# Optimization experiments

Hardware: AMD Instinct MI355X
Metric: run time of the kernel (lower is better)

## Reference

```python
import jax, jax.numpy as jnp
import numpy as np

OFFSET_SCALE = 6.0
H = W = 256


def setup_inputs() -> dict:
    key = jax.random.key(0)
    k1, k2, k3, k4 = jax.random.split(key, 4)
    B = 128
    Offset = jax.random.normal(k1, (B, 3, H, W), dtype=jnp.float32) * 0.05
    Posmap_kpt = jax.random.normal(k2, (B, 3, H, W), dtype=jnp.float32)
    mean_posmap = jax.random.normal(k3, (3, H, W), dtype=jnp.float32)
    uv_kpt = jax.random.randint(k4, (68, 2), 0, H)
    return {"Offset": Offset, "Posmap_kpt": Posmap_kpt,
            "mean_posmap": mean_posmap, "uv_kpt": uv_kpt}


def _safe_norm(d):
    # row-wise L2 norm with zero-safe gradient (row 0 of d is exactly zero)
    sq = jnp.sum(d * d, axis=1)
    pos = sq > 0
    return jnp.where(pos, jnp.sqrt(jnp.where(pos, sq, 1.0)), 0.0)


def _kabsch(src, dst):
    # src, dst: [68, 3] -> similarity transform (scaled R [3,3], t [3])
    s1 = jnp.sum(_safe_norm(src - src[0]))
    s2 = jnp.sum(_safe_norm(dst - dst[0]))
    scale = s2 / s1
    A = src * scale
    AA = A - A.mean(axis=0)
    BB = dst - dst.mean(axis=0)
    Hm = AA.T @ BB                        # [3,3] cross-covariance
    U, S, Vh = jnp.linalg.svd(Hm, full_matrices=False)
    R = Vh.T @ U.T                        # torch.svd returns V, so R = V U^T
    t = jnp.mean(dst - A @ R.T, axis=0)
    return R * scale, t


def reference(Offset, Posmap_kpt, mean_posmap, uv_kpt):
    B = Offset.shape[0]
    offsetmap = (Offset * OFFSET_SCALE + mean_posmap).transpose(0, 2, 3, 1)  # [B,H,W,3]
    kptmap = Posmap_kpt.transpose(0, 2, 3, 1)                                # [B,H,W,3]
    kpt_dst = kptmap[:, uv_kpt[:, 0], uv_kpt[:, 1]]                          # [B,68,3]
    kpt_src = offsetmap[:, uv_kpt[:, 0], uv_kpt[:, 1]]                       # [B,68,3]
    offsetflat = offsetmap.reshape(B, H * W, 3)                              # [B,65536,3]
    R, t = jax.vmap(_kabsch)(kpt_src, kpt_dst)                               # [B,3,3], [B,3]
    outpos = jnp.einsum('bnd,bed->bne', offsetflat, R) + t[:, None, :]       # x @ R^T + t
    return outpos.reshape(B, H, W, 3).transpose(0, 3, 1, 2)
```

## Files before the change

### kernel.cpp

```cpp
#include <hip/hip_runtime.h>

#define HW (256*256)
#define NKPT 68
#define NB 128

typedef float v4f __attribute__((ext_vector_type(4)));

__device__ inline void inv3x3(const double m[9], double inv[9], double* detOut) {
    double c00 =  m[4]*m[8] - m[5]*m[7];
    double c01 = -(m[3]*m[8] - m[5]*m[6]);
    double c02 =  m[3]*m[7] - m[4]*m[6];
    double det = m[0]*c00 + m[1]*c01 + m[2]*c02;
    double id = 1.0 / det;
    inv[0] = c00 * id;
    inv[1] = (m[2]*m[7] - m[1]*m[8]) * id;
    inv[2] = (m[1]*m[5] - m[2]*m[4]) * id;
    inv[3] = c01 * id;
    inv[4] = (m[0]*m[8] - m[2]*m[6]) * id;
    inv[5] = (m[2]*m[3] - m[0]*m[5]) * id;
    inv[6] = c02 * id;
    inv[7] = (m[1]*m[6] - m[0]*m[7]) * id;
    inv[8] = (m[0]*m[4] - m[1]*m[3]) * id;
    *detOut = det;
}

__global__ __launch_bounds__(128) void kabsch_kernel(
    const float* __restrict__ Offset,
    const float* __restrict__ Posmap,
    const float* __restrict__ meanp,
    const int*   __restrict__ uv,
    float* __restrict__ RT)
{
    const int b   = blockIdx.x;
    const int tid = threadIdx.x;
    __shared__ double red[17][NKPT];
    __shared__ double res[17];

    if (tid < NKPT) {
        const int r  = uv[2*tid],   c  = uv[2*tid+1];
        const int r0 = uv[0],       c0 = uv[1];
        const int p  = r  * 256 + c;
        const int p0 = r0 * 256 + c0;
        const float* offB = Offset + (size_t)b * 3 * HW;
        const float* posB = Posmap + (size_t)b * 3 * HW;
        double s[3], d[3], s0[3], d0[3];
        #pragma unroll
        for (int k = 0; k < 3; ++k) {
            s[k]  = (double)offB[k*HW + p ] * 6.0 + (double)meanp[k*HW + p ];
            d[k]  = (double)posB[k*HW + p ];
            s0[k] = (double)offB[k*HW + p0] * 6.0 + (double)meanp[k*HW + p0];
            d0[k] = (double)posB[k*HW + p0];
        }
        int q = 0;
        #pragma unroll
        for (int k = 0; k < 3; ++k) red[q++][tid] = s[k];
        #pragma unroll
        for (int k = 0; k < 3; ++k) red[q++][tid] = d[k];
        #pragma unroll
        for (int i = 0; i < 3; ++i)
            #pragma unroll
            for (int j = 0; j < 3; ++j) red[q++][tid] = s[i] * d[j];
        double ns2 = 0.0, nd2 = 0.0;
        #pragma unroll
        for (int k = 0; k < 3; ++k) {
            double e = s[k] - s0[k]; ns2 += e*e;
            double f = d[k] - d0[k]; nd2 += f*f;
        }
        red[q++][tid] = (ns2 > 0.0) ? sqrt(ns2) : 0.0;
        red[q++][tid] = (nd2 > 0.0) ? sqrt(nd2) : 0.0;
    }
    __syncthreads();
    if (tid < 17) {
        double acc = 0.0;
        for (int i = 0; i < NKPT; ++i) acc += red[tid][i];
        res[tid] = acc;
    }
    __syncthreads();
    if (tid == 0) {
        const double sumS[3] = {res[0], res[1], res[2]};
        const double sumD[3] = {res[3], res[4], res[5]};
        double cross[9];
        #pragma unroll
        for (int k = 0; k < 9; ++k) cross[k] = res[6+k];
        const double s1 = res[15], s2 = res[16];
        const double scale = s2 / s1;
        double mS[3], mD[3];
        #pragma unroll
        for (int k = 0; k < 3; ++k) { mS[k] = sumS[k] / NKPT; mD[k] = sumD[k] / NKPT; }
        double Wm[9];
        #pragma unroll
        for (int i = 0; i < 3; ++i)
            #pragma unroll
            for (int j = 0; j < 3; ++j)
                Wm[i*3+j] = scale * (cross[i*3+j] - (double)NKPT * mS[i] * mD[j]);
        for (int it = 0; it < 8; ++it) {
            double inv[9], det;
            inv3x3(Wm, inv, &det);
            double g  = cbrt(fabs(det));
            double gi = 1.0 / g;
            double Wn[9];
            #pragma unroll
            for (int r = 0; r < 3; ++r)
                #pragma unroll
                for (int c = 0; c < 3; ++c)
                    Wn[r*3+c] = 0.5 * (gi * Wm[r*3+c] + g * inv[c*3+r]);
            #pragma unroll
            for (int k = 0; k < 9; ++k) Wm[k] = Wn[k];
        }
        float* o = RT + b * 12;
        #pragma unroll
        for (int e = 0; e < 3; ++e)
            #pragma unroll
            for (int d = 0; d < 3; ++d)
                o[e*3+d] = (float)(scale * Wm[d*3+e]);
        #pragma unroll
        for (int e = 0; e < 3; ++e) {
            double acc = mD[e];
            #pragma unroll
            for (int d = 0; d < 3; ++d) acc -= scale * mS[d] * Wm[d*3+e];
            o[9+e] = (float)acc;
        }
    }
}

__global__ __launch_bounds__(256) void apply_kernel(
    const float* __restrict__ Offset,
    const float* __restrict__ meanp,
    const float* __restrict__ RT,
    float* __restrict__ out)
{
    const int blk  = blockIdx.x;
    const int b    = blk >> 4;
    const int slab = blk & 15;
    const int p0   = slab * 4096 + threadIdx.x * 4;

    const float* rt = RT + b * 12;
    const float r00 = rt[0], r01 = rt[1], r02 = rt[2];
    const float r10 = rt[3], r11 = rt[4], r12 = rt[5];
    const float r20 = rt[6], r21 = rt[7], r22 = rt[8];
    const float t0  = rt[9], t1  = rt[10], t2 = rt[11];

    const size_t bbase = (size_t)b * 3 * HW;

    v4f a[3][4], m[3][4];
    #pragma unroll
    for (int g = 0; g < 4; ++g) {
        const int p = p0 + g * 1024;
        #pragma unroll
        for (int ch = 0; ch < 3; ++ch)
            a[ch][g] = __builtin_nontemporal_load((const v4f*)(Offset + bbase + (size_t)ch * HW + p));
    }
    #pragma unroll
    for (int g = 0; g < 4; ++g) {
        const int p = p0 + g * 1024;
        #pragma unroll
        for (int ch = 0; ch < 3; ++ch)
            m[ch][g] = *(const v4f*)(meanp + (size_t)ch * HW + p);
    }

    #pragma unroll
    for (int g = 0; g < 4; ++g) {
        const int p = p0 + g * 1024;
        v4f o0, o1, o2;
        #pragma unroll
        for (int L = 0; L < 4; ++L) {
            float x = fmaf(6.0f, a[0][g][L], m[0][g][L]);
            float y = fmaf(6.0f, a[1][g][L], m[1][g][L]);
            float z = fmaf(6.0f, a[2][g][L], m[2][g][L]);
            o0[L] = fmaf(r00, x, fmaf(r01, y, fmaf(r02, z, t0)));
            o1[L] = fmaf(r10, x, fmaf(r11, y, fmaf(r12, z, t1)));
            o2[L] = fmaf(r20, x, fmaf(r21, y, fmaf(r22, z, t2)));
        }
        __builtin_nontemporal_store(o0, (v4f*)(out + bbase + 0*HW + p));
        __builtin_nontemporal_store(o1, (v4f*)(out + bbase + 1*HW + p));
        __builtin_nontemporal_store(o2, (v4f*)(out + bbase + 2*HW + p));
    }
}

extern "C" void kernel_launch(void* const* d_in, const int* in_sizes, int n_in,
                              void* d_out, int out_size, void* d_ws, size_t ws_size,
                              hipStream_t stream) {
    const float* Offset = (const float*)d_in[0];
    const float* Posmap = (const float*)d_in[1];
    const float* meanp  = (const float*)d_in[2];
    const int*   uv     = (const int*)d_in[3];
    float* out = (float*)d_out;
    float* RT  = (float*)d_ws;

    kabsch_kernel<<<NB, 128, 0, stream>>>(Offset, Posmap, meanp, uv, RT);
    apply_kernel<<<NB * 16, 256, 0, stream>>>(Offset, meanp, RT, out);
}
```

Before: 225.3 us.

## Fuse Kabsch solve into apply kernel, recomputing transform per block

Merges the per-batch Kabsch kernel and the apply kernel into one launch. Each of the 2048 blocks redundantly gathers the 68 keypoints and runs the double-precision reduction and polar iteration, then applies the transform from shared memory. This removes a kernel launch, the dependency gap between launches, and the global round trip of the transform. The cost is 16x redundant serial FP64 work on one thread per block before the streaming phase starts.

```diff
diff --git a/kernel.cpp b/kernel.cpp
--- a/kernel.cpp
+++ b/kernel.cpp
@@ -24,25 +24,30 @@
     *detOut = det;
 }
 
-__global__ __launch_bounds__(128) void kabsch_kernel(
+__global__ __launch_bounds__(256) void fused_kernel(
     const float* __restrict__ Offset,
     const float* __restrict__ Posmap,
     const float* __restrict__ meanp,
     const int*   __restrict__ uv,
-    float* __restrict__ RT)
+    float* __restrict__ out)
 {
-    const int b   = blockIdx.x;
-    const int tid = threadIdx.x;
+    const int b    = blockIdx.x & 127;
+    const int slab = blockIdx.x >> 7;
+    const int tid  = threadIdx.x;
+
     __shared__ double red[17][NKPT];
     __shared__ double res[17];
+    __shared__ float  rtS[12];
+
+    const size_t bbase = (size_t)b * 3 * HW;
 
     if (tid < NKPT) {
         const int r  = uv[2*tid],   c  = uv[2*tid+1];
         const int r0 = uv[0],       c0 = uv[1];
         const int p  = r  * 256 + c;
         const int p0 = r0 * 256 + c0;
-        const float* offB = Offset + (size_t)b * 3 * HW;
-        const float* posB = Posmap + (size_t)b * 3 * HW;
+        const float* offB = Offset + bbase;
+        const float* posB = Posmap + bbase;
         double s[3], d[3], s0[3], d0[3];
         #pragma unroll
         for (int k = 0; k < 3; ++k) {
@@ -76,6 +81,7 @@
         res[tid] = acc;
     }
     __syncthreads();
+
     if (tid == 0) {
         const double sumS[3] = {res[0], res[1], res[2]};
         const double sumD[3] = {res[3], res[4], res[5]};
@@ -107,40 +113,27 @@
             #pragma unroll
             for (int k = 0; k < 9; ++k) Wm[k] = Wn[k];
         }
-        float* o = RT + b * 12;
         #pragma unroll
         for (int e = 0; e < 3; ++e)
             #pragma unroll
             for (int d = 0; d < 3; ++d)
-                o[e*3+d] = (float)(scale * Wm[d*3+e]);
+                rtS[e*3+d] = (float)(scale * Wm[d*3+e]);
         #pragma unroll
         for (int e = 0; e < 3; ++e) {
             double acc = mD[e];
             #pragma unroll
             for (int d = 0; d < 3; ++d) acc -= scale * mS[d] * Wm[d*3+e];
-            o[9+e] = (float)acc;
+            rtS[9+e] = (float)acc;
         }
     }
-}
+    __syncthreads();
 
-__global__ __launch_bounds__(256) void apply_kernel(
-    const float* __restrict__ Offset,
-    const float* __restrict__ meanp,
-    const float* __restrict__ RT,
-    float* __restrict__ out)
-{
-    const int blk  = blockIdx.x;
-    const int b    = blk >> 4;
-    const int slab = blk & 15;
-    const int p0   = slab * 4096 + threadIdx.x * 4;
+    const float r00 = rtS[0], r01 = rtS[1], r02 = rtS[2];
+    const float r10 = rtS[3], r11 = rtS[4], r12 = rtS[5];
+    const float r20 = rtS[6], r21 = rtS[7], r22 = rtS[8];
+    const float t0  = rtS[9], t1  = rtS[10], t2 = rtS[11];
 
-    const float* rt = RT + b * 12;
-    const float r00 = rt[0], r01 = rt[1], r02 = rt[2];
-    const float r10 = rt[3], r11 = rt[4], r12 = rt[5];
-    const float r20 = rt[6], r21 = rt[7], r22 = rt[8];
-    const float t0  = rt[9], t1  = rt[10], t2 = rt[11];
-
-    const size_t bbase = (size_t)b * 3 * HW;
+    const int p0 = slab * 4096 + tid * 4;
 
     v4f a[3][4], m[3][4];
     #pragma unroll
@@ -185,8 +178,6 @@
     const float* meanp  = (const float*)d_in[2];
     const int*   uv     = (const int*)d_in[3];
     float* out = (float*)d_out;
-    float* RT  = (float*)d_ws;
 
-    kabsch_kernel<<<NB, 128, 0, stream>>>(Offset, Posmap, meanp, uv, RT);
-    apply_kernel<<<NB * 16, 256, 0, stream>>>(Offset, meanp, RT, out);
+    fused_kernel<<<NB * 16, 256, 0, stream>>>(Offset, Posmap, meanp, uv, out);
 }
```

After: 229.2 us. Within noise of the previous version (+1.7%).
